# Kernel tuning notes

Measured on AMD Instinct MI355X. Metric: run time of the kernel, lower is better.

## Reference

```python
import jax, jax.numpy as jnp
import numpy as np


def _unfold(x, ks, pad):
    # torch nn.Unfold ordering: flattened channel dim is (c, kh, kw), output (b, c*ks*ks, h*w)
    b, c, h, w = x.shape
    if ks == 1:
        return x.reshape(b, c, h * w)
    xp = jnp.pad(x, ((0, 0), (0, 0), (pad, pad), (pad, pad)))
    patches = jnp.stack([xp[:, :, i:i + h, j:j + w] for i in range(ks) for j in range(ks)], axis=2)  # (b,c,ks*ks,h,w)
    return patches.reshape(b, c * ks * ks, h * w)


def _cg_conv(x, weight, ce_w, gd_w, gd2_w, ci_w, ks, pad, g=8):
    # Content-gated conv: SE-style dynamic kernel generation + unfold + batched matmul
    b, c, h, w = x.shape
    oc = weight.shape[0]
    # AdaptiveMaxPool2d((ks,ks)); h,w divisible by ks so bins are uniform
    gl = x.reshape(b, c, ks, h // ks, ks, w // ks).max(axis=(3, 5)).reshape(b, c, ks * ks)
    ce2 = jnp.einsum('bck,nk->bcn', gl, ce_w)                      # (b,c,num_lat)
    out = jnp.einsum('bcn,kn->bck', jax.nn.relu(ce2), gd_w)        # (b,c,ks*ks)
    # channel path: (b,c//g,g,num_lat) -> transpose -> Linear(g -> oc/(c//g))
    t = jax.nn.relu(jnp.transpose(ce2.reshape(b, c // g, g, -1), (0, 1, 3, 2)))
    ocp = jnp.transpose(jnp.einsum('bpng,og->bpno', t, ci_w), (0, 1, 3, 2)).reshape(b, oc, -1)
    ocp = jnp.einsum('bon,kn->bok', jax.nn.relu(ocp), gd2_w)       # (b,oc,ks*ks)
    dyn = jax.nn.sigmoid(out[:, None, :, :] + ocp[:, :, None, :])  # (b,oc,c,ks*ks)
    dyn = dyn * weight.reshape(1, oc, c, ks * ks)
    x_un = _unfold(x, ks, pad)                                     # (b, c*ks*ks, h*w)
    y = jnp.einsum('bok,bkl->bol', dyn.reshape(b, oc, c * ks * ks), x_un)
    return y.reshape(b, oc, h, w)


def setup_inputs() -> dict:
    key = jax.random.key(0)
    ks_ = jax.random.split(key, 12)
    b, c_in, c_hid, c_out, H, W = 4, 64, 256, 64, 96, 96
    s = 0.02
    inp = {
        'x': jax.random.normal(ks_[0], (b, c_in, H, W), jnp.float32),
        # fc1: 1x1, num_lat = 1, ci: 8 -> 256//(64//8)=32
        'fc1_weight': jax.random.normal(ks_[1], (c_hid, c_in, 1, 1), jnp.float32) * s,
        'fc1_ce': jax.random.normal(ks_[2], (1, 1), jnp.float32) * s,
        'fc1_gd': jax.random.normal(ks_[3], (1, 1), jnp.float32) * s,
        'fc1_gd2': jax.random.normal(ks_[4], (1, 1), jnp.float32) * s,
        'fc1_ci': jax.random.normal(ks_[5], (32, 8), jnp.float32) * s,
        # fc2: 3x3, num_lat = 5, ci: 8 -> 64//(256//8)=2
        'fc2_weight': jax.random.normal(ks_[6], (c_out, c_hid, 3, 3), jnp.float32) * s,
        'fc2_ce': jax.random.normal(ks_[7], (5, 9), jnp.float32) * s,
        'fc2_gd': jax.random.normal(ks_[8], (9, 5), jnp.float32) * s,
        'fc2_gd2': jax.random.normal(ks_[9], (9, 5), jnp.float32) * s,
        'fc2_ci': jax.random.normal(ks_[10], (2, 8), jnp.float32) * s,
    }
    return inp


def reference(x, fc1_weight, fc1_ce, fc1_gd, fc1_gd2, fc1_ci,
              fc2_weight, fc2_ce, fc2_gd, fc2_gd2, fc2_ci):
    h = _cg_conv(x, fc1_weight, fc1_ce, fc1_gd, fc1_gd2, fc1_ci, ks=1, pad=0)
    h = jax.nn.gelu(h, approximate=False)  # torch nn.GELU default is exact erf
    return _cg_conv(h, fc2_weight, fc2_ce, fc2_gd, fc2_gd2, fc2_ci, ks=3, pad=1)
```

## Files before the change

kernel.cpp:

```cpp
#include <hip/hip_runtime.h>
#include <math.h>

typedef __attribute__((ext_vector_type(8))) short short8x;
typedef __attribute__((ext_vector_type(4))) float float4x;
typedef unsigned short u16;
typedef unsigned int u32;

__device__ __forceinline__ float bf2f(u16 u) {
    return __uint_as_float(((u32)u) << 16);
}
__device__ __forceinline__ u16 f2bf(float f) {
    u32 u = __float_as_uint(f);
    u32 r = (u + 0x7fffu + ((u >> 16) & 1u)) >> 16;
    return (u16)r;
}
__device__ __forceinline__ u32 fenc(float f) {
    u32 b = __float_as_uint(f);
    return b ^ (0x80000000u | (u32)((int)b >> 31));
}
__device__ __forceinline__ float fdec(u32 u) {
    u32 b = (u & 0x80000000u) ? (u ^ 0x80000000u) : ~u;
    return __uint_as_float(b);
}


__global__ __launch_bounds__(256) void k_gl1(const float* __restrict__ x, float* __restrict__ gl1,
                                             u32* __restrict__ h2p32, u32* __restrict__ gl2u) {
    if (blockIdx.x >= 256) {
        int t = threadIdx.x;
        int plane_id = blockIdx.x - 256;
        u32* plane = h2p32 + plane_id * (98 * 98 * 16);
        for (int i = t; i < 1568; i += 256) plane[i] = 0u;
        for (int i = t; i < 1568; i += 256) plane[97 * 98 * 16 + i] = 0u;
        for (int i = t; i < 3072; i += 256) {
            int r = (i >> 5) + 1;
            int p = ((i >> 4) & 1) * 97;
            int w = i & 15;
            plane[(r * 98 + p) * 16 + w] = 0u;
        }
        for (int i = plane_id * 288 + t; i < (plane_id + 1) * 288; i += 256)
            gl2u[i] = 0u;
        return;
    }
    int b = blockIdx.x >> 6, c = blockIdx.x & 63;
    const float4* p = (const float4*)(x + (b * 64 + c) * 9216);
    float m = -1e30f;
    #pragma unroll
    for (int i = 0; i < 9; i++) {
        float4 v = p[i * 256 + threadIdx.x];
        m = fmaxf(m, fmaxf(fmaxf(v.x, v.y), fmaxf(v.z, v.w)));
    }
    __shared__ float red[256];
    red[threadIdx.x] = m;
    __syncthreads();
    for (int s = 128; s > 0; s >>= 1) {
        if (threadIdx.x < s) red[threadIdx.x] = fmaxf(red[threadIdx.x], red[threadIdx.x + s]);
        __syncthreads();
    }
    if (threadIdx.x == 0) gl1[b * 64 + c] = red[0];
}

__global__ __launch_bounds__(256) void k_gate1(const float* __restrict__ gl1,
                                               const float* __restrict__ ce, const float* __restrict__ gd,
                                               const float* __restrict__ gd2, const float* __restrict__ ci,
                                               const float* __restrict__ w1, u16* __restrict__ W1A) {
    int b = blockIdx.x >> 4, s = blockIdx.x & 15;
    int t = threadIdx.x;
    __shared__ float rce[64], out1[64], ocp[256];
    float cew = ce[0], gdw = gd[0], gd2w = gd2[0];
    if (t < 64) {
        float r = fmaxf(gl1[b * 64 + t] * cew, 0.f);
        rce[t] = r;
        out1[t] = r * gdw;
    }
    __syncthreads();
    {
        int p = t >> 5, oi = t & 31;
        float sv = 0.f;
        #pragma unroll
        for (int g = 0; g < 8; g++) sv += rce[p * 8 + g] * ci[oi * 8 + g];
        ocp[t] = fmaxf(sv, 0.f) * gd2w;
    }
    __syncthreads();
    u16* Wb = W1A + b * 256 * 64;
    #pragma unroll
    for (int i = 0; i < 4; i++) {
        int idx = s * 1024 + i * 256 + t;
        int o = idx >> 6, c = idx & 63;
        float v = out1[c] + ocp[o];
        float sg = 1.f / (1.f + expf(-v));
        Wb[idx] = f2bf(sg * w1[idx]);
    }
}

__global__ __launch_bounds__(256) void k_gemm1(const u16* __restrict__ W1A, const float* __restrict__ x,
                                               u16* __restrict__ h2p, u32* __restrict__ gl2u) {
    int bi = blockIdx.x;
    int b = bi / 192, rem = bi % 192;
    int y = rem >> 1, half = rem & 1;
    int t = threadIdx.x, wave = t >> 6, lane = t & 63, l15 = lane & 15, quad = lane >> 4;

    __shared__ __align__(16) u16 xs[48 * 72];
    const float* xb = x + (b * 64) * 9216 + y * 96 + half * 48;
    #pragma unroll
    for (int i = 0; i < 12; i++) {
        int idx = i * 256 + t;
        int c = idx / 48, px = idx - c * 48;
        xs[px * 72 + c] = f2bf(xb[c * 9216 + px]);
    }
    __syncthreads();

    float4x acc[4][3];
    #pragma unroll
    for (int mt = 0; mt < 4; mt++)
        #pragma unroll
        for (int nt = 0; nt < 3; nt++) acc[mt][nt] = (float4x){0.f, 0.f, 0.f, 0.f};
    const u16* Wb = W1A + b * 256 * 64;
    #pragma unroll
    for (int c0 = 0; c0 < 64; c0 += 32) {
        short8x bfr[3];
        #pragma unroll
        for (int nt = 0; nt < 3; nt++)
            bfr[nt] = *(const short8x*)(xs + (nt * 16 + l15) * 72 + c0 + quad * 8);
        #pragma unroll
        for (int mt = 0; mt < 4; mt++) {
            int oc = wave * 64 + mt * 16 + l15;
            short8x afr = *(const short8x*)(Wb + oc * 64 + c0 + quad * 8);
            #pragma unroll
            for (int nt = 0; nt < 3; nt++)
                acc[mt][nt] = __builtin_amdgcn_mfma_f32_16x16x32_bf16(afr, bfr[nt], acc[mt][nt], 0, 0, 0);
        }
    }
    const float is2 = 0.70710678118654752f;
    float gf[4][3][4];
    #pragma unroll
    for (int mt = 0; mt < 4; mt++) {
        #pragma unroll
        for (int nt = 0; nt < 3; nt++) {
            int xx = half * 48 + nt * 16 + l15;
            int oc0 = wave * 64 + mt * 16 + quad * 4;
            int g = oc0 >> 5, cl = oc0 & 31;
            u16 pk[4];
            #pragma unroll
            for (int r = 0; r < 4; r++) {
                float v = acc[mt][nt][r];
                float gl = 0.5f * v * (1.f + erff(v * is2));
                gf[mt][nt][r] = gl;
                pk[r] = f2bf(gl);
            }
            u16* dst = h2p + ((((b * 8 + g) * 98 + y + 1) * 98) + xx + 1) * 32 + cl;
            *(ushort4*)dst = make_ushort4(pk[0], pk[1], pk[2], pk[3]);
        }
    }
    int ki = y >> 5;
    int kA = ki * 3 + (half == 0 ? 0 : 1);
    int kB = ki * 3 + (half == 0 ? 1 : 2);
    #pragma unroll
    for (int mt = 0; mt < 4; mt++) {
        float vA[4], vB[4];
        #pragma unroll
        for (int r = 0; r < 4; r++) {
            if (half == 0) { vA[r] = fmaxf(gf[mt][0][r], gf[mt][1][r]); vB[r] = gf[mt][2][r]; }
            else           { vA[r] = gf[mt][0][r]; vB[r] = fmaxf(gf[mt][1][r], gf[mt][2][r]); }
        }
        #pragma unroll
        for (int m = 1; m < 16; m <<= 1) {
            #pragma unroll
            for (int r = 0; r < 4; r++) {
                vA[r] = fmaxf(vA[r], __shfl_xor(vA[r], m));
                vB[r] = fmaxf(vB[r], __shfl_xor(vB[r], m));
            }
        }
        if (l15 == 0) {
            #pragma unroll
            for (int r = 0; r < 4; r++) {
                int oc = wave * 64 + mt * 16 + quad * 4 + r;
                atomicMax(&gl2u[(b * 9 + kA) * 256 + oc], fenc(vA[r]));
                atomicMax(&gl2u[(b * 9 + kB) * 256 + oc], fenc(vB[r]));
            }
        }
    }
}

__global__ __launch_bounds__(256) void k_gate2(const u32* __restrict__ gl2u,
                                               const float* __restrict__ ce, const float* __restrict__ gd,
                                               const float* __restrict__ gd2, const float* __restrict__ ci,
                                               const float* __restrict__ w2, u16* __restrict__ W2A) {
    int b = blockIdx.x >> 4, s = blockIdx.x & 15;
    int t = threadIdx.x;
    __shared__ float rce[256][5];
    __shared__ float out2[256][9];
    __shared__ float ocp2[64][9];
    {
        float gl[9];
        #pragma unroll
        for (int k = 0; k < 9; k++) gl[k] = fdec(gl2u[(b * 9 + k) * 256 + t]);
        float r[5];
        #pragma unroll
        for (int n = 0; n < 5; n++) {
            float sv = 0.f;
            #pragma unroll
            for (int k = 0; k < 9; k++) sv += gl[k] * ce[n * 9 + k];
            r[n] = fmaxf(sv, 0.f);
            rce[t][n] = r[n];
        }
        #pragma unroll
        for (int k = 0; k < 9; k++) {
            float sv = 0.f;
            #pragma unroll
            for (int n = 0; n < 5; n++) sv += r[n] * gd[k * 5 + n];
            out2[t][k] = sv;
        }
    }
    __syncthreads();
    if (t < 64) {
        int p = t >> 1, oi = t & 1;
        float rt[5];
        #pragma unroll
        for (int n = 0; n < 5; n++) {
            float sv = 0.f;
            #pragma unroll
            for (int g = 0; g < 8; g++) sv += rce[p * 8 + g][n] * ci[oi * 8 + g];
            rt[n] = fmaxf(sv, 0.f);
        }
        #pragma unroll
        for (int k = 0; k < 9; k++) {
            float sv = 0.f;
            #pragma unroll
            for (int n = 0; n < 5; n++) sv += rt[n] * gd2[k * 5 + n];
            ocp2[t][k] = sv;
        }
    }
    __syncthreads();
    u16* Wb = W2A + b * (8 * 9 * 64 * 32);
    for (int it = 0; it < 36; it++) {
        int flat = s * 9216 + it * 256 + t;
        int cl = flat & 31;
        int o = (flat >> 5) & 63;
        int rest = flat >> 11;
        int k = rest % 9, g = rest / 9;
        int c = g * 32 + cl;
        float v = out2[c][k] + ocp2[o][k];
        float sg = 1.f / (1.f + expf(-v));
        Wb[flat] = f2bf(sg * w2[(o * 256 + c) * 9 + k]);
    }
}

__global__ __launch_bounds__(256) void k_conv2(const u16* __restrict__ W2A, const u16* __restrict__ h2p,
                                               float* __restrict__ out) {
    int bi = blockIdx.x;
    int b = bi / 192, rem = bi % 192;
    int y = rem >> 1, half = rem & 1;
    int t = threadIdx.x, wave = t >> 6, lane = t & 63, l15 = lane & 15, quad = lane >> 4;
    __shared__ __align__(16) u16 Bls[3 * 50 * 32];
    float4x acc[3];
    #pragma unroll
    for (int nt = 0; nt < 3; nt++) acc[nt] = (float4x){0.f, 0.f, 0.f, 0.f};

    for (int g = 0; g < 8; g++) {
        __syncthreads();
        const u16* plane = h2p + (b * 8 + g) * (98 * 98 * 32);
        for (int i = t; i < 600; i += 256) {
            int r = i / 200, c16 = i - r * 200;
            const uint4* src = (const uint4*)(plane + ((y + r) * 98 + half * 48) * 32 + c16 * 8);
            ((uint4*)Bls)[r * 200 + c16] = *src;
        }
        __syncthreads();
        const u16* Wg = W2A + (b * 8 + g) * (9 * 64 * 32);
        #pragma unroll
        for (int k = 0; k < 9; k++) {
            int ki = k / 3, kj = k - ki * 3;
            short8x af = *(const short8x*)(Wg + (k * 64 + wave * 16 + l15) * 32 + quad * 8);
            #pragma unroll
            for (int nt = 0; nt < 3; nt++) {
                int pxl = nt * 16 + l15 + kj;
                short8x bf = *(const short8x*)(Bls + (ki * 50 + pxl) * 32 + quad * 8);
                acc[nt] = __builtin_amdgcn_mfma_f32_16x16x32_bf16(af, bf, acc[nt], 0, 0, 0);
            }
        }
    }
    #pragma unroll
    for (int nt = 0; nt < 3; nt++) {
        int xx = half * 48 + nt * 16 + l15;
        #pragma unroll
        for (int r = 0; r < 4; r++) {
            int oc = wave * 16 + quad * 4 + r;
            out[((b * 64 + oc) * 96 + y) * 96 + xx] = acc[nt][r];
        }
    }
}

extern "C" void kernel_launch(void* const* d_in, const int* in_sizes, int n_in,
                              void* d_out, int out_size, void* d_ws, size_t ws_size,
                              hipStream_t stream) {
    const float* x    = (const float*)d_in[0];
    const float* w1   = (const float*)d_in[1];
    const float* ce1  = (const float*)d_in[2];
    const float* gd1  = (const float*)d_in[3];
    const float* gd21 = (const float*)d_in[4];
    const float* ci1  = (const float*)d_in[5];
    const float* w2   = (const float*)d_in[6];
    const float* ce2  = (const float*)d_in[7];
    const float* gd2  = (const float*)d_in[8];
    const float* gd22 = (const float*)d_in[9];
    const float* ci2  = (const float*)d_in[10];
    float* out = (float*)d_out;

    char* ws = (char*)d_ws;
    u16*   h2p  = (u16*)(ws + 4718592);
    u16*   W1A  = (u16*)(ws + 24387584);
    u16*   W2A  = (u16*)(ws + 24518656);
    float* gl1  = (float*)(ws + 25698304);
    u32*   gl2u = (u32*)(ws + 25796608);

    k_gl1  <<<288, 256, 0, stream>>>(x, gl1, (u32*)h2p, gl2u);
    k_gate1<<<64,  256, 0, stream>>>(gl1, ce1, gd1, gd21, ci1, w1, W1A);
    k_gemm1<<<768, 256, 0, stream>>>(W1A, x, h2p, gl2u);
    k_gate2<<<64,  256, 0, stream>>>(gl2u, ce2, gd2, gd22, ci2, w2, W2A);
    k_conv2<<<768, 256, 0, stream>>>(W2A, h2p, out);
}
```

Before: 137.8 us.

## Double-buffer conv2 LDS tiles with register prefetch and vectorize gemm1 input loads

The conv2 kernel now keeps two LDS buffers and prefetches the next channel group's input rows into registers while MFMAs run on the current group, then stores them into the alternate buffer. This removes one barrier per group and hides global load latency behind compute. The gemm1 staging loop also reads x as float2 pairs instead of scalar floats, halving the number of load instructions. The cost is doubled LDS use in conv2 and more live registers, which may lower occupancy.

Measured after the change: 132.2 us (median of 2 runs). 4.1% less time.

```diff
diff --git a/kernel.cpp b/kernel.cpp
--- a/kernel.cpp
+++ b/kernel.cpp
@@ -102,11 +102,15 @@
 
     __shared__ __align__(16) u16 xs[48 * 72];
     const float* xb = x + (b * 64) * 9216 + y * 96 + half * 48;
-    #pragma unroll
-    for (int i = 0; i < 12; i++) {
+    const float2* xb2 = (const float2*)xb;
+    #pragma unroll
+    for (int i = 0; i < 6; i++) {
         int idx = i * 256 + t;
-        int c = idx / 48, px = idx - c * 48;
-        xs[px * 72 + c] = f2bf(xb[c * 9216 + px]);
+        int c = idx / 24, px2 = idx - c * 24;
+        float2 v = xb2[c * 4608 + px2];
+        int px = px2 * 2;
+        xs[px * 72 + c] = f2bf(v.x);
+        xs[(px + 1) * 72 + c] = f2bf(v.y);
     }
     __syncthreads();
 
@@ -252,21 +256,42 @@
     int b = bi / 192, rem = bi % 192;
     int y = rem >> 1, half = rem & 1;
     int t = threadIdx.x, wave = t >> 6, lane = t & 63, l15 = lane & 15, quad = lane >> 4;
-    __shared__ __align__(16) u16 Bls[3 * 50 * 32];
+    __shared__ __align__(16) u16 Bls[2][3 * 50 * 32];
+
+    int offs[3];
+    #pragma unroll
+    for (int j = 0; j < 3; j++) {
+        int i = t + j * 256;
+        int r = i / 200, c16 = i - r * 200;
+        offs[j] = ((y + r) * 98 + half * 48) * 32 + c16 * 8;
+    }
+    const int plane_sz = 98 * 98 * 32;
+    uint4 p0, p1, p2;
+    {
+        const u16* pl = h2p + (b * 8) * plane_sz;
+        p0 = *(const uint4*)(pl + offs[0]);
+        p1 = *(const uint4*)(pl + offs[1]);
+        if (t < 88) p2 = *(const uint4*)(pl + offs[2]);
+        uint4* Bd = (uint4*)Bls[0];
+        Bd[t] = p0;
+        Bd[t + 256] = p1;
+        if (t < 88) Bd[t + 512] = p2;
+    }
+
     float4x acc[3];
     #pragma unroll
     for (int nt = 0; nt < 3; nt++) acc[nt] = (float4x){0.f, 0.f, 0.f, 0.f};
 
     for (int g = 0; g < 8; g++) {
         __syncthreads();
-        const u16* plane = h2p + (b * 8 + g) * (98 * 98 * 32);
-        for (int i = t; i < 600; i += 256) {
-            int r = i / 200, c16 = i - r * 200;
-            const uint4* src = (const uint4*)(plane + ((y + r) * 98 + half * 48) * 32 + c16 * 8);
-            ((uint4*)Bls)[r * 200 + c16] = *src;
-        }
-        __syncthreads();
+        if (g < 7) {
+            const u16* pl = h2p + (b * 8 + g + 1) * plane_sz;
+            p0 = *(const uint4*)(pl + offs[0]);
+            p1 = *(const uint4*)(pl + offs[1]);
+            if (t < 88) p2 = *(const uint4*)(pl + offs[2]);
+        }
         const u16* Wg = W2A + (b * 8 + g) * (9 * 64 * 32);
+        const u16* Bcur = Bls[g & 1];
         #pragma unroll
         for (int k = 0; k < 9; k++) {
             int ki = k / 3, kj = k - ki * 3;
@@ -274,9 +299,15 @@
             #pragma unroll
             for (int nt = 0; nt < 3; nt++) {
                 int pxl = nt * 16 + l15 + kj;
-                short8x bf = *(const short8x*)(Bls + (ki * 50 + pxl) * 32 + quad * 8);
+                short8x bf = *(const short8x*)(Bcur + (ki * 50 + pxl) * 32 + quad * 8);
                 acc[nt] = __builtin_amdgcn_mfma_f32_16x16x32_bf16(af, bf, acc[nt], 0, 0, 0);
             }
+        }
+        if (g < 7) {
+            uint4* Bd = (uint4*)Bls[(g + 1) & 1];
+            Bd[t] = p0;
+            Bd[t + 256] = p1;
+            if (t < 88) Bd[t + 512] = p2;
         }
     }
     #pragma unroll
```
